# Optimization experiments

Measured on AMD Instinct MI355X. Metric: run time of the kernel, lower is better.

Reference implementation:

```python
import jax, jax.numpy as jnp
import numpy as np

F = 26          # number of sparse fields
V = 100000      # vocab per field
D = 32          # embedding dim
DENSE = 13
HID = (1024, 512, 256)
B = 16384


def setup_inputs() -> dict:
    key = jax.random.key(0)
    ks = jax.random.split(key, 16)
    x_sparse = jax.random.randint(ks[0], (B, F), 0, V, dtype=jnp.int32)
    x_dense = jax.random.normal(ks[1], (B, DENSE), dtype=jnp.float32)
    emb_tables = jax.random.normal(ks[2], (F, V, D), dtype=jnp.float32) * 0.05
    lin_tables = jax.random.normal(ks[3], (F, V), dtype=jnp.float32) * 0.05
    dnn_in = F * D + DENSE
    dims = (dnn_in,) + HID
    params = {}
    for i in range(len(HID)):
        params[f'W{i}'] = jax.random.normal(ks[4 + i], (dims[i], dims[i + 1]), dtype=jnp.float32) * (1.0 / np.sqrt(dims[i]))
        params[f'b{i}'] = jnp.zeros((dims[i + 1],), dtype=jnp.float32)
    Wout = jax.random.normal(ks[10], (HID[-1], 1), dtype=jnp.float32) * (1.0 / np.sqrt(HID[-1]))
    bout = jnp.zeros((1,), dtype=jnp.float32)
    return dict(x_sparse=x_sparse, x_dense=x_dense, emb_tables=emb_tables,
                lin_tables=lin_tables,
                W0=params['W0'], b0=params['b0'],
                W1=params['W1'], b1=params['b1'],
                W2=params['W2'], b2=params['b2'],
                Wout=Wout, bout=bout)


def reference(x_sparse, x_dense, emb_tables, lin_tables,
              W0, b0, W1, b1, W2, b2, Wout, bout):
    f_idx = jnp.arange(F)[None, :]            # [1, F]
    # batched multi-field gather: [B, F, D] and [B, F]
    emb = emb_tables[f_idx, x_sparse]          # [B, F, D]
    lin = lin_tables[f_idx, x_sparse]          # [B, F]
    linear_logit = lin.sum(axis=1)             # [B]
    # FM pairwise sum_{i<j} <e_i, e_j> via sum-square identity
    s = emb.sum(axis=1)                        # [B, D]
    fm_logit = 0.5 * ((s * s).sum(axis=-1) - (emb * emb).sum(axis=(1, 2)))  # [B]
    # DNN on concatenated embeddings + dense feats
    h = jnp.concatenate([emb.reshape(emb.shape[0], F * D), x_dense], axis=1)
    h = jax.nn.relu(h @ W0 + b0)
    h = jax.nn.relu(h @ W1 + b1)
    h = jax.nn.relu(h @ W2 + b2)
    dnn_logit = (h @ Wout + bout)[:, 0]        # [B]
    return jax.nn.sigmoid(linear_logit + fm_logit + dnn_logit)
```

## Files before the change

kernel.cpp:

```cpp
#include <hip/hip_runtime.h>
#include <math.h>


typedef __attribute__((ext_vector_type(8))) short shortx8;
typedef __attribute__((ext_vector_type(4))) float floatx4;

#define AS1 __attribute__((address_space(1)))
#define AS3 __attribute__((address_space(3)))

__device__ __forceinline__ void load_lds_16(const void* g, void* l) {
    __builtin_amdgcn_global_load_lds((AS1 void*)g, (AS3 void*)l, 16, 0, 0);
}

__device__ __forceinline__ unsigned short f2bf(float x) {
    union { float f; unsigned int u; } v; v.f = x;
    unsigned int r = v.u + 0x7fffu + ((v.u >> 16) & 1u);
    return (unsigned short)(r >> 16);
}

template<int N>
__device__ __forceinline__ void waitvm() {
    asm volatile("s_waitcnt vmcnt(%0)" :: "n"(N) : "memory");
}

__device__ __forceinline__ void bar() {
    asm volatile("" ::: "memory");
    __builtin_amdgcn_s_barrier();
    asm volatile("" ::: "memory");
}

__device__ __forceinline__
void wtrans_tile(const float* __restrict__ W, unsigned short* __restrict__ Wt,
                 int K, int N, int Kpad, int bx, int by, int tid)
{
    __shared__ float tile[32][33];
    const int k0 = bx * 32, n0 = by * 32;
    const int tx = tid & 31, ty = tid >> 5;
#pragma unroll
    for (int i = 0; i < 32; i += 8) {
        int k = k0 + ty + i;
        tile[ty + i][tx] = (k < K) ? W[(size_t)k * N + (n0 + tx)] : 0.f;
    }
    __syncthreads();
#pragma unroll
    for (int i = 0; i < 32; i += 8) {
        int n = n0 + ty + i, kk = k0 + tx;
        Wt[(size_t)n * Kpad + kk] = f2bf(tile[tx][ty + i]);
    }
}

__global__ __launch_bounds__(256)
void prep(const int* __restrict__ xs, const float* __restrict__ xd,
          const float* __restrict__ emb, const float* __restrict__ lint,
          const float* __restrict__ W0, const float* __restrict__ W1,
          const float* __restrict__ W2,
          unsigned short* __restrict__ h0, float* __restrict__ lg,
          unsigned short* __restrict__ Wt0, unsigned short* __restrict__ Wt1,
          unsigned short* __restrict__ Wt2)
{
    const int bid = blockIdx.x;
    const int tid = threadIdx.x;

    if (bid >= 4096) {
        int t = bid - 4096;
        if (t < 896)       wtrans_tile(W0, Wt0, 845, 1024, 896, t % 28, t / 28, tid);
        else if (t < 1408) wtrans_tile(W1, Wt1, 1024, 512, 1024, (t - 896) % 32, (t - 896) / 32, tid);
        else               wtrans_tile(W2, Wt2, 512, 256, 512, (t - 1408) % 16, (t - 1408) / 16, tid);
        return;
    }

    const int lane = tid & 63;
    const int wave = tid >> 6;
    const int b = bid * 4 + wave;

    int idx = 0; float linv = 0.f;
    if (lane < 26) {
        idx = xs[b * 26 + lane];
        linv = lint[(size_t)lane * 100000 + idx];
    }
    const int d = lane & 31;
    const int half = lane >> 5;
    float s = 0.f, sq = 0.f;
    unsigned short* hrow = h0 + (size_t)b * 896;
#pragma unroll
    for (int it = 0; it < 13; ++it) {
        int f = it * 2 + half;
        int fidx = __shfl(idx, f);
        float v = emb[((size_t)f * 100000 + (size_t)fidx) * 32 + d];
        s += v; sq += v * v;
        hrow[f * 32 + d] = f2bf(v);
    }
    s += __shfl_xor(s, 32);
    float t = 0.25f * s * s - 0.5f * sq + linv;
#pragma unroll
    for (int off = 32; off >= 1; off >>= 1) t += __shfl_xor(t, off);
    if (lane == 0) lg[b] = t;

    if (lane < 13) hrow[832 + lane] = f2bf(xd[b * 13 + lane]);
    else           hrow[832 + lane] = 0;
}

template<int BM, int BN>
__global__ __launch_bounds__(512, 2)
void gemm_pipe(const unsigned short* __restrict__ X,
               const unsigned short* __restrict__ Wt,
               const float* __restrict__ bias,
               unsigned short* __restrict__ Y,
               int M, int N, int K, int nby)
{
    constexpr int CA  = BM / 128;
    constexpr int CB  = BN / 128;
    constexpr int LPT = CA + CB;
    constexpr int MR  = BM / 32;
    constexpr int NR  = BN / 64;

    __shared__ alignas(16) unsigned short As[4][BM * 32];
    __shared__ alignas(16) unsigned short Bs[4][BN * 32];

    const int tid   = threadIdx.x;
    const int lane  = tid & 63;
    const int wave  = tid >> 6;
    const int lrow  = lane & 15;
    const int lquad = lane >> 4;
    const int wm = (wave >> 2) * (BM / 2);
    const int wn = (wave & 3) * (BN / 4);

    const int nwg = gridDim.x;
    const int bid = blockIdx.x;
    const int swz = (bid & 7) * (nwg >> 3) + (bid >> 3);
    const int bx = swz / nby, by = swz % nby;
    const int bm = bx * BM, bn = by * BN;

    floatx4 acc[MR][NR];
    const floatx4 z4 = {0.f, 0.f, 0.f, 0.f};
#pragma unroll
    for (int i = 0; i < MR; ++i)
#pragma unroll
        for (int j = 0; j < NR; ++j) acc[i][j] = z4;

    const int NT = K >> 5;

    auto STAGE = [&](int tt) {
        const int k0 = tt << 5;
        unsigned short* a_dst = As[tt & 3];
        unsigned short* b_dst = Bs[tt & 3];
#pragma unroll
        for (int q = 0; q < CA; ++q) {
            int c = tid + q * 512;
            int row = c >> 2, sl = c & 3;
            load_lds_16(X + (size_t)(bm + row) * K + (k0 + ((sl ^ (row & 3)) << 3)),
                        a_dst + c * 8);
        }
#pragma unroll
        for (int q = 0; q < CB; ++q) {
            int c = tid + q * 512;
            int row = c >> 2, sl = c & 3;
            load_lds_16(Wt + (size_t)(bn + row) * K + (k0 + ((sl ^ (row & 3)) << 3)),
                        b_dst + c * 8);
        }
    };

    STAGE(0); STAGE(1); STAGE(2);

    const int abase = (wm + lrow) * 32 + ((lquad ^ (lrow & 3)) << 3);
    const int bbase = (wn + lrow) * 32 + ((lquad ^ (lrow & 3)) << 3);

    for (int t = 0; t < NT; ++t) {
        const int cur = t & 3;
        if (t + 3 < NT)      { STAGE(t + 3); waitvm<3 * LPT>(); }
        else if (t + 2 < NT) waitvm<2 * LPT>();
        else if (t + 1 < NT) waitvm<LPT>();
        else                 waitvm<0>();
        bar();

        shortx8 a[MR], b[NR];
#pragma unroll
        for (int i = 0; i < MR; ++i)
            a[i] = *(const shortx8*)(&As[cur][abase + i * 512]);
#pragma unroll
        for (int j = 0; j < NR; ++j)
            b[j] = *(const shortx8*)(&Bs[cur][bbase + j * 512]);

        __builtin_amdgcn_s_setprio(1);
#pragma unroll
        for (int i = 0; i < MR; ++i)
#pragma unroll
            for (int j = 0; j < NR; ++j)
                acc[i][j] = __builtin_amdgcn_mfma_f32_16x16x32_bf16(a[i], b[j], acc[i][j], 0, 0, 0);
        __builtin_amdgcn_s_setprio(0);
        bar();
    }

#pragma unroll
    for (int i = 0; i < MR; ++i) {
        const int row = bm + wm + i * 16 + lquad * 4;
#pragma unroll
        for (int j = 0; j < NR; ++j) {
            const int col = bn + wn + j * 16 + lrow;
            const float bv = bias[col];
#pragma unroll
            for (int r = 0; r < 4; ++r) {
                float v = fmaxf(acc[i][j][r] + bv, 0.f);
                Y[(size_t)(row + r) * N + col] = f2bf(v);
            }
        }
    }
}

__global__ __launch_bounds__(256)
void gemm3_final(const unsigned short* __restrict__ X,
                 const unsigned short* __restrict__ Wt,
                 const float* __restrict__ bias,
                 const float* __restrict__ Wo,
                 const float* __restrict__ bo,
                 const float* __restrict__ lg,
                 float* __restrict__ out)
{
    const int K = 512;
    __shared__ alignas(16) unsigned short As[64 * 32];
    __shared__ alignas(16) unsigned short Bs[256 * 32];
    __shared__ float red[4][64];

    const int tid  = threadIdx.x;
    const int lane = tid & 63;
    const int wave = tid >> 6;
    const int bm = blockIdx.x * 64;
    const int wn = wave * 64;
    const int lrow  = lane & 15;
    const int lquad = lane >> 4;

    floatx4 acc[4][4];
    const floatx4 z4 = {0.f, 0.f, 0.f, 0.f};
#pragma unroll
    for (int i = 0; i < 4; ++i)
#pragma unroll
        for (int j = 0; j < 4; ++j) acc[i][j] = z4;

    const int ar = tid >> 2, akp = (tid & 3) << 3;

    for (int k0 = 0; k0 < K; k0 += 32) {
        load_lds_16(X + (size_t)(bm + ar) * K + (k0 + akp), As + (size_t)tid * 8);
#pragma unroll
        for (int q = 0; q < 4; ++q) {
            int c = tid + q * 256;
            load_lds_16(Wt + (size_t)(c >> 2) * K + (k0 + akp), Bs + (size_t)c * 8);
        }
        __syncthreads();

        shortx8 a[4], b[4];
#pragma unroll
        for (int i = 0; i < 4; ++i)
            a[i] = *(const shortx8*)(As + (i * 16 + lrow) * 32 + lquad * 8);
#pragma unroll
        for (int j = 0; j < 4; ++j)
            b[j] = *(const shortx8*)(Bs + (wn + j * 16 + lrow) * 32 + lquad * 8);
#pragma unroll
        for (int i = 0; i < 4; ++i)
#pragma unroll
            for (int j = 0; j < 4; ++j)
                acc[i][j] = __builtin_amdgcn_mfma_f32_16x16x32_bf16(a[i], b[j], acc[i][j], 0, 0, 0);
        __syncthreads();
    }

    float bv[4], wv[4];
#pragma unroll
    for (int j = 0; j < 4; ++j) {
        int col = wn + j * 16 + lrow;
        bv[j] = bias[col];
        wv[j] = Wo[col];
    }
#pragma unroll
    for (int i = 0; i < 4; ++i) {
#pragma unroll
        for (int r = 0; r < 4; ++r) {
            float p = 0.f;
#pragma unroll
            for (int j = 0; j < 4; ++j) {
                float v = fmaxf(acc[i][j][r] + bv[j], 0.f);
                p += v * wv[j];
            }
            p += __shfl_xor(p, 1);
            p += __shfl_xor(p, 2);
            p += __shfl_xor(p, 4);
            p += __shfl_xor(p, 8);
            if (lrow == 0) red[wave][i * 16 + lquad * 4 + r] = p;
        }
    }
    __syncthreads();
    if (tid < 64) {
        float s = red[0][tid] + red[1][tid] + red[2][tid] + red[3][tid];
        float x = s + bo[0] + lg[bm + tid];
        out[bm + tid] = 1.f / (1.f + expf(-x));
    }
}

extern "C" void kernel_launch(void* const* d_in, const int* in_sizes, int n_in,
                              void* d_out, int out_size, void* d_ws, size_t ws_size,
                              hipStream_t stream)
{
    const int*   xs = (const int*)d_in[0];
    const float* xd = (const float*)d_in[1];
    const float* em = (const float*)d_in[2];
    const float* li = (const float*)d_in[3];
    const float* W0 = (const float*)d_in[4];
    const float* b0 = (const float*)d_in[5];
    const float* W1 = (const float*)d_in[6];
    const float* b1 = (const float*)d_in[7];
    const float* W2 = (const float*)d_in[8];
    const float* b2 = (const float*)d_in[9];
    const float* Wo = (const float*)d_in[10];
    const float* bo = (const float*)d_in[11];
    float* out = (float*)d_out;

    char* ws = (char*)d_ws;
    unsigned short* h0  = (unsigned short*)(ws);
    unsigned short* h1  = (unsigned short*)(ws + 29360128);
    unsigned short* h2  = (unsigned short*)(ws);
    unsigned short* Wt0 = (unsigned short*)(ws + 62914560);
    unsigned short* Wt1 = (unsigned short*)(ws + 64749568);
    unsigned short* Wt2 = (unsigned short*)(ws + 65798144);
    float*          lg  = (float*)(ws + 66060288);

    prep<<<5632, 256, 0, stream>>>(xs, xd, em, li, W0, W1, W2, h0, lg, Wt0, Wt1, Wt2);

    gemm_pipe<256, 256><<<256, 512, 0, stream>>>(h0, Wt0, b0, h1, 16384, 1024, 896, 4);
    gemm_pipe<128, 256><<<256, 512, 0, stream>>>(h1, Wt1, b1, h2, 16384, 512, 1024, 2);
    gemm3_final<<<256, 256, 0, stream>>>(h2, Wt2, b2, Wo, bo, lg, out);
}
```

Before: 498.1 us.

## Retile GEMM kernels to 256-thread blocks with 3-stage pipeline and swizzled LDS

The pipelined GEMM moves from 512-thread 4-stage blocks to 256-thread blocks with a 2x2 wave layout. Each wave now computes a larger 64x128 sub-tile, and the ring drops to 3 stages with a 2-deep prefetch. The first GEMM shrinks from 256x256 to 128x256 tiles, and the grid becomes a 2D launch without the L2 block swizzle. The final GEMM gets an XOR-swizzled LDS layout to reduce bank conflicts. The trade is more register pressure per wave and shallower latency hiding, plus possible loss of L2 locality from dropping the swizzle.

```diff
diff --git a/kernel.cpp b/kernel.cpp
--- a/kernel.cpp
+++ b/kernel.cpp
@@ -101,35 +101,31 @@
 }
 
 template<int BM, int BN>
-__global__ __launch_bounds__(512, 2)
+__global__ __launch_bounds__(256, 2)
 void gemm_pipe(const unsigned short* __restrict__ X,
                const unsigned short* __restrict__ Wt,
                const float* __restrict__ bias,
                unsigned short* __restrict__ Y,
-               int M, int N, int K, int nby)
-{
-    constexpr int CA  = BM / 128;
-    constexpr int CB  = BN / 128;
+               int M, int N, int K)
+{
+    constexpr int CA  = BM / 64;
+    constexpr int CB  = BN / 64;
     constexpr int LPT = CA + CB;
     constexpr int MR  = BM / 32;
-    constexpr int NR  = BN / 64;
-
-    __shared__ alignas(16) unsigned short As[4][BM * 32];
-    __shared__ alignas(16) unsigned short Bs[4][BN * 32];
+    constexpr int NR  = BN / 32;
+
+    __shared__ alignas(16) unsigned short As[3][BM * 32];
+    __shared__ alignas(16) unsigned short Bs[3][BN * 32];
 
     const int tid   = threadIdx.x;
     const int lane  = tid & 63;
     const int wave  = tid >> 6;
     const int lrow  = lane & 15;
     const int lquad = lane >> 4;
-    const int wm = (wave >> 2) * (BM / 2);
-    const int wn = (wave & 3) * (BN / 4);
-
-    const int nwg = gridDim.x;
-    const int bid = blockIdx.x;
-    const int swz = (bid & 7) * (nwg >> 3) + (bid >> 3);
-    const int bx = swz / nby, by = swz % nby;
-    const int bm = bx * BM, bn = by * BN;
+    const int wm = (wave & 1) * (BM / 2);
+    const int wn = (wave >> 1) * (BN / 2);
+    const int bm = blockIdx.x * BM;
+    const int bn = blockIdx.y * BN;
 
     floatx4 acc[MR][NR];
     const floatx4 z4 = {0.f, 0.f, 0.f, 0.f};
@@ -142,33 +138,32 @@
 
     auto STAGE = [&](int tt) {
         const int k0 = tt << 5;
-        unsigned short* a_dst = As[tt & 3];
-        unsigned short* b_dst = Bs[tt & 3];
+        unsigned short* a_dst = As[tt % 3];
+        unsigned short* b_dst = Bs[tt % 3];
 #pragma unroll
         for (int q = 0; q < CA; ++q) {
-            int c = tid + q * 512;
+            int c = tid + q * 256;
             int row = c >> 2, sl = c & 3;
             load_lds_16(X + (size_t)(bm + row) * K + (k0 + ((sl ^ (row & 3)) << 3)),
                         a_dst + c * 8);
         }
 #pragma unroll
         for (int q = 0; q < CB; ++q) {
-            int c = tid + q * 512;
+            int c = tid + q * 256;
             int row = c >> 2, sl = c & 3;
             load_lds_16(Wt + (size_t)(bn + row) * K + (k0 + ((sl ^ (row & 3)) << 3)),
                         b_dst + c * 8);
         }
     };
 
-    STAGE(0); STAGE(1); STAGE(2);
+    STAGE(0); STAGE(1);
 
     const int abase = (wm + lrow) * 32 + ((lquad ^ (lrow & 3)) << 3);
     const int bbase = (wn + lrow) * 32 + ((lquad ^ (lrow & 3)) << 3);
 
     for (int t = 0; t < NT; ++t) {
-        const int cur = t & 3;
-        if (t + 3 < NT)      { STAGE(t + 3); waitvm<3 * LPT>(); }
-        else if (t + 2 < NT) waitvm<2 * LPT>();
+        const int cur = t % 3;
+        if (t + 2 < NT)      { STAGE(t + 2); waitvm<2 * LPT>(); }
         else if (t + 1 < NT) waitvm<LPT>();
         else                 waitvm<0>();
         bar();
@@ -236,24 +231,28 @@
 #pragma unroll
         for (int j = 0; j < 4; ++j) acc[i][j] = z4;
 
-    const int ar = tid >> 2, akp = (tid & 3) << 3;
+    const int ar = tid >> 2;
+    const int asw = ((tid & 3) ^ (ar & 3)) << 3;
 
     for (int k0 = 0; k0 < K; k0 += 32) {
-        load_lds_16(X + (size_t)(bm + ar) * K + (k0 + akp), As + (size_t)tid * 8);
+        load_lds_16(X + (size_t)(bm + ar) * K + (k0 + asw), As + (size_t)tid * 8);
 #pragma unroll
         for (int q = 0; q < 4; ++q) {
             int c = tid + q * 256;
-            load_lds_16(Wt + (size_t)(c >> 2) * K + (k0 + akp), Bs + (size_t)c * 8);
+            int row = c >> 2;
+            load_lds_16(Wt + (size_t)row * K + (k0 + (((c & 3) ^ (row & 3)) << 3)),
+                        Bs + (size_t)c * 8);
         }
         __syncthreads();
 
+        const int rsw = (lquad ^ (lrow & 3)) << 3;
         shortx8 a[4], b[4];
 #pragma unroll
         for (int i = 0; i < 4; ++i)
-            a[i] = *(const shortx8*)(As + (i * 16 + lrow) * 32 + lquad * 8);
+            a[i] = *(const shortx8*)(As + (i * 16 + lrow) * 32 + rsw);
 #pragma unroll
         for (int j = 0; j < 4; ++j)
-            b[j] = *(const shortx8*)(Bs + (wn + j * 16 + lrow) * 32 + lquad * 8);
+            b[j] = *(const shortx8*)(Bs + (wn + j * 16 + lrow) * 32 + rsw);
 #pragma unroll
         for (int i = 0; i < 4; ++i)
 #pragma unroll
@@ -323,7 +322,7 @@
 
     prep<<<5632, 256, 0, stream>>>(xs, xd, em, li, W0, W1, W2, h0, lg, Wt0, Wt1, Wt2);
 
-    gemm_pipe<256, 256><<<256, 512, 0, stream>>>(h0, Wt0, b0, h1, 16384, 1024, 896, 4);
-    gemm_pipe<128, 256><<<256, 512, 0, stream>>>(h1, Wt1, b1, h2, 16384, 512, 1024, 2);
+    gemm_pipe<128, 256><<<dim3(128, 4), 256, 0, stream>>>(h0, Wt0, b0, h1, 16384, 1024, 896);
+    gemm_pipe<128, 256><<<dim3(128, 2), 256, 0, stream>>>(h1, Wt1, b1, h2, 16384, 512, 1024);
     gemm3_final<<<256, 256, 0, stream>>>(h2, Wt2, b2, Wo, bo, lg, out);
 }
```

After: 497.4 us. About the same (-0.2%).
